# Performance work log

Hardware: AMD Instinct MI355X
Metric: run time of the kernel (lower is better)

## Reference

```python
import jax, jax.numpy as jnp
import numpy as np

N = 100_000      # nodes
E = 1_600_000    # directed edges (avg degree 16)
F_IN = 128       # num_node_features
H = 8            # heads in conv1
C = 32           # hidden_channels
G = 64           # graphs in batch
NC = 10          # num_classes


def setup_inputs() -> dict:
    key = jax.random.key(0)
    ks = jax.random.split(key, 12)
    gl = lambda k, shape, fan: (jax.random.normal(k, shape, jnp.float32) / np.sqrt(fan)).astype(jnp.float32)
    return {
        "x": jax.random.normal(ks[0], (N, F_IN), jnp.float32),
        "edge_index": jax.random.randint(ks[1], (2, E), 0, N, dtype=jnp.int32),
        "batch": jnp.sort(jax.random.randint(ks[2], (N,), 0, G, dtype=jnp.int32)),
        "W1": gl(ks[3], (F_IN, H * C), F_IN),
        "att_src1": gl(ks[4], (H, C), C),
        "att_dst1": gl(ks[5], (H, C), C),
        "b1": jnp.zeros((H * C,), jnp.float32),
        "W2": gl(ks[6], (H * C, C), H * C),
        "att_src2": gl(ks[7], (1, C), C),
        "att_dst2": gl(ks[8], (1, C), C),
        "b2": jnp.zeros((C,), jnp.float32),
        "Wlin": gl(ks[9], (C, NC), C),
        "blin": jnp.zeros((NC,), jnp.float32),
    }


def gat_conv(x, src, dst, W, att_src, att_dst, bias, heads, ch, concat):
    """PyG GATConv (eval mode): gather, LeakyReLU(0.2) scores, segment softmax over dst, scatter-sum."""
    n = x.shape[0]
    h = (x @ W).reshape(n, heads, ch)                     # [N,H,C]
    a_s = jnp.sum(h * att_src, axis=-1)                   # [N,H]
    a_d = jnp.sum(h * att_dst, axis=-1)                   # [N,H]
    e = jax.nn.leaky_relu(a_s[src] + a_d[dst], 0.2)       # [E,H]
    m = jax.ops.segment_max(e, dst, num_segments=n)       # [N,H], stable softmax
    p = jnp.exp(e - m[dst])
    z = jax.ops.segment_sum(p, dst, num_segments=n)
    coef = p / (z[dst] + 1e-16)                           # [E,H]
    out = jax.ops.segment_sum(coef[:, :, None] * h[src], dst, num_segments=n)  # [N,H,C]
    out = out.reshape(n, heads * ch) if concat else out.mean(axis=1)
    return out + bias


def reference(x, edge_index, batch, W1, att_src1, att_dst1, b1,
              W2, att_src2, att_dst2, b2, Wlin, blin):
    n = x.shape[0]
    loops = jnp.arange(n, dtype=edge_index.dtype)         # GATConv add_self_loops=True
    src = jnp.concatenate([edge_index[0], loops])
    dst = jnp.concatenate([edge_index[1], loops])

    h = gat_conv(x, src, dst, W1, att_src1, att_dst1, b1, H, C, concat=True)
    h = jax.nn.elu(h)                                     # dropout is identity in eval
    h = gat_conv(h, src, dst, W2, att_src2, att_dst2, b2, 1, C, concat=False)

    # global_mean_pool over graph ids
    sums = jax.ops.segment_sum(h, batch, num_segments=G)  # [G,C]
    cnts = jax.ops.segment_sum(jnp.ones((n,), h.dtype), batch, num_segments=G)
    pooled = sums / jnp.maximum(cnts, 1.0)[:, None]

    return pooled @ Wlin + blin                           # [G,NC]
```

## Files before the change

kernel.cpp:

```cpp
#include <hip/hip_runtime.h>
#include <cstdint>

#define NN 100000
#define EE 1600000
#define GG 64
#define FIN 128
#define HC 256
#define NC 10

typedef short v8s __attribute__((ext_vector_type(8)));
typedef float v4f __attribute__((ext_vector_type(4)));

static __device__ __forceinline__ float lrelu(float x) { return x > 0.f ? x : 0.2f * x; }
static __device__ __forceinline__ float bf2f(unsigned short b) {
  return __uint_as_float(((unsigned int)b) << 16);
}
static __device__ __forceinline__ unsigned short f2bf(float f) {
  unsigned int u = __float_as_uint(f);
  unsigned int r = (u + 0x7FFFu + ((u >> 16) & 1u)) >> 16;
  return (unsigned short)r;
}
static __device__ __forceinline__ void unpack2(unsigned int u, float& f0, float& f1) {
  f0 = __uint_as_float(u << 16);
  f1 = __uint_as_float(u & 0xFFFF0000u);
}

__global__ __launch_bounds__(256) void k_prep(const int* __restrict__ ei,
                                              int* __restrict__ counts,
                                              const float* __restrict__ W1,
                                              unsigned short* __restrict__ W1tg,
                                              const float* __restrict__ W2,
                                              unsigned short* __restrict__ W2thi,
                                              unsigned short* __restrict__ W2tlo) {
  const int b = blockIdx.x;
  const int t = threadIdx.x;
  if (b < 6250) {
    const int idx = b * 256 + t;
    atomicAdd(&counts[ei[EE + idx]], 1);
  } else if (b < 6506) {
    const int n = b - 6250;
    if (t < 128) W1tg[n * 128 + t] = f2bf(W1[t * HC + n]);
  } else {
    const int oc = b - 6506;
    float wv = W2[t * 32 + oc];
    unsigned short hi = f2bf(wv);
    W2thi[oc * 256 + t] = hi;
    W2tlo[oc * 256 + t] = f2bf(wv - bf2f(hi));
  }
}

__global__ __launch_bounds__(256) void k_gemm1(const float* __restrict__ x,
                                               const unsigned short* __restrict__ W1tg,
                                               const float* __restrict__ att_src1,
                                               const float* __restrict__ att_dst1,
                                               unsigned short* __restrict__ h1b,
                                               float* __restrict__ as1,
                                               float* __restrict__ ad1) {
  const int t = threadIdx.x;
  const int m0 = blockIdx.x * 64;
  const int n0 = blockIdx.y * 128;
  const int hb = blockIdx.y * 4;
  const int lane = t & 63;
  const int wm = t >> 6;
  const int ml = lane & 15;
  const int quad = lane >> 4;
  int row = m0 + wm * 16 + ml; if (row >= NN) row = NN - 1;
  v4f acc[8];
#pragma unroll
  for (int tt = 0; tt < 8; ++tt) acc[tt] = (v4f){0.f, 0.f, 0.f, 0.f};
#pragma unroll
  for (int kk = 0; kk < 4; ++kk) {
    const int k0 = kk * 32 + quad * 8;
    const float4 xa = *(const float4*)(x + (size_t)row * FIN + k0);
    const float4 xc = *(const float4*)(x + (size_t)row * FIN + k0 + 4);
    v8s a;
    a[0] = (short)f2bf(xa.x); a[1] = (short)f2bf(xa.y);
    a[2] = (short)f2bf(xa.z); a[3] = (short)f2bf(xa.w);
    a[4] = (short)f2bf(xc.x); a[5] = (short)f2bf(xc.y);
    a[6] = (short)f2bf(xc.z); a[7] = (short)f2bf(xc.w);
#pragma unroll
    for (int tt = 0; tt < 8; ++tt) {
      v8s b = *(const v8s*)(W1tg + (size_t)(n0 + tt * 16 + ml) * FIN + k0);
      acc[tt] = __builtin_amdgcn_mfma_f32_16x16x32_bf16(a, b, acc[tt], 0, 0, 0);
    }
  }
#pragma unroll
  for (int tt = 0; tt < 8; ++tt) {
#pragma unroll
    for (int r = 0; r < 4; ++r) {
      int rg = m0 + wm * 16 + quad * 4 + r;
      if (rg < NN) h1b[(size_t)rg * HC + n0 + tt * 16 + ml] = f2bf(acc[tt][r]);
    }
  }
  float ps[4][4], pd[4][4];
#pragma unroll
  for (int i = 0; i < 4; ++i)
#pragma unroll
    for (int r = 0; r < 4; ++r) { ps[i][r] = 0.f; pd[i][r] = 0.f; }
#pragma unroll
  for (int i = 0; i < 4; ++i) {
#pragma unroll
    for (int half = 0; half < 2; ++half) {
      const int tt = 2 * i + half;
      const float a_s = att_src1[(hb + i) * 32 + half * 16 + ml];
      const float a_d = att_dst1[(hb + i) * 32 + half * 16 + ml];
#pragma unroll
      for (int r = 0; r < 4; ++r) {
        ps[i][r] += acc[tt][r] * a_s;
        pd[i][r] += acc[tt][r] * a_d;
      }
    }
  }
#pragma unroll
  for (int i = 0; i < 4; ++i) {
#pragma unroll
    for (int r = 0; r < 4; ++r) {
      float s = ps[i][r], d = pd[i][r];
      s += __shfl_xor(s, 1, 64); s += __shfl_xor(s, 2, 64);
      s += __shfl_xor(s, 4, 64); s += __shfl_xor(s, 8, 64);
      d += __shfl_xor(d, 1, 64); d += __shfl_xor(d, 2, 64);
      d += __shfl_xor(d, 4, 64); d += __shfl_xor(d, 8, 64);
      ps[i][r] = s; pd[i][r] = d;
    }
  }
  if (ml == 0) {
#pragma unroll
    for (int r = 0; r < 4; ++r) {
      int rg = m0 + wm * 16 + quad * 4 + r;
      if (rg < NN) {
#pragma unroll
        for (int i = 0; i < 4; ++i) {
          as1[rg * 8 + hb + i] = ps[i][r];
          ad1[rg * 8 + hb + i] = pd[i][r];
        }
      }
    }
  }
}

__global__ void k_scan1(const int* __restrict__ counts, int* __restrict__ offs,
                        int* __restrict__ bsums) {
  __shared__ int s[256];
  const int t = threadIdx.x;
  const int i = blockIdx.x * 256 + t;
  int v = (i < NN) ? counts[i] : 0;
  s[t] = v;
  __syncthreads();
  for (int off = 1; off < 256; off <<= 1) {
    int tv = (t >= off) ? s[t - off] : 0;
    __syncthreads();
    s[t] += tv;
    __syncthreads();
  }
  if (i < NN) offs[i] = s[t] - v;
  if (t == 255) bsums[blockIdx.x] = s[255];
}

__global__ void k_scan2(int* __restrict__ bsums, int nb) {
  __shared__ int s[512];
  const int t = threadIdx.x;
  int v = (t < nb) ? bsums[t] : 0;
  s[t] = v;
  __syncthreads();
  for (int off = 1; off < 512; off <<= 1) {
    int tv = (t >= off) ? s[t - off] : 0;
    __syncthreads();
    s[t] += tv;
    __syncthreads();
  }
  if (t < nb) bsums[t] = s[t] - v;
}

__global__ void k_scan3(int* __restrict__ offs, const int* __restrict__ bsums,
                        int* __restrict__ cursor, int* __restrict__ esrc) {
  const int i = blockIdx.x * 256 + threadIdx.x;
  if (i < NN) {
    int v = offs[i] + bsums[i >> 8];
    offs[i] = v;
    cursor[i] = v;
  }
  if (i == 0) offs[NN] = EE;
  if (blockIdx.x == 0 && threadIdx.x < 16) esrc[EE + threadIdx.x] = 0;
}

__global__ void k_scatter(const int* __restrict__ ei, int* __restrict__ cursor,
                          int* __restrict__ esrc) {
  int e = blockIdx.x * 256 + threadIdx.x;
  if (e < EE) {
    int s = ei[e];
    int d = ei[EE + e];
    int p = atomicAdd(&cursor[d], 1);
    esrc[p] = s;
  }
}

__global__ __launch_bounds__(512) void k_agg1(const unsigned short* __restrict__ h1b,
                                              const float* __restrict__ as1,
                                              const float* __restrict__ ad1,
                                              const int* __restrict__ offs,
                                              const int* __restrict__ esrc,
                                              const float* __restrict__ b1,
                                              const unsigned short* __restrict__ W2thi,
                                              const unsigned short* __restrict__ W2tlo,
                                              const float* __restrict__ att_src2,
                                              const float* __restrict__ att_dst2,
                                              unsigned short* __restrict__ h2b,
                                              float* __restrict__ as2,
                                              float* __restrict__ ad2) {
  __shared__ float wl[8][8][36];
  __shared__ __attribute__((aligned(16))) unsigned short o1hi[8][272];
  __shared__ __attribute__((aligned(16))) unsigned short o1lo[8][272];
  const int t = threadIdx.x;
  const int lane = t & 63;
  const int w = t >> 6;
  const int n0 = blockIdx.x * 8;
  const int nu = __builtin_amdgcn_readfirstlane(n0 + w);
  const int hl = lane & 31;
  const int half = lane >> 5;
  const int head = lane >> 3;
  const uint2* __restrict__ h1u2 = (const uint2*)h1b;
  const int start = offs[nu], end = offs[nu + 1];
  const float4 dnA = *(const float4*)(ad1 + (size_t)nu * 8);
  const float4 dnB = *(const float4*)(ad1 + (size_t)nu * 8 + 4);
  const float4 dn4 = (lane & 32) ? dnB : dnA;

  float z, a0, a1, a2, a3;
  {
    float w0 = __expf(lrelu(as1[nu * 8 + head] + ad1[nu * 8 + head]));
    uint2 q = h1u2[(size_t)nu * 64 + lane];
    float f0, f1, f2, f3; unpack2(q.x, f0, f1); unpack2(q.y, f2, f3);
    z = w0; a0 = w0 * f0; a1 = w0 * f1; a2 = w0 * f2; a3 = w0 * f3;
  }
  for (int base = start; base < end; base += 32) {
    const int cnt = min(32, end - base);
    int s = 0;
    if (hl < cnt) s = esrc[base + hl];
    const int hb4 = half << 2;
    const float4 av = *(const float4*)(as1 + (size_t)s * 8 + hb4);
    float w0 = __expf(lrelu(av.x + dn4.x));
    float w1 = __expf(lrelu(av.y + dn4.y));
    float w2 = __expf(lrelu(av.z + dn4.z));
    float w3 = __expf(lrelu(av.w + dn4.w));
    const bool act = hl < cnt;
    wl[w][hb4 + 0][hl] = act ? w0 : 0.f;
    wl[w][hb4 + 1][hl] = act ? w1 : 0.f;
    wl[w][hb4 + 2][hl] = act ? w2 : 0.f;
    wl[w][hb4 + 3][hl] = act ? w3 : 0.f;
    const int cnt4 = (cnt + 3) & ~3;
    int jb = 0;
    for (; jb + 8 <= cnt4; jb += 8) {
      uint2 q[8];
#pragma unroll
      for (int u = 0; u < 8; ++u) {
        const int sj = esrc[base + jb + u];
        q[u] = h1u2[(size_t)sj * 64 + lane];
      }
      const float4 wq0 = *(const float4*)&wl[w][head][jb];
      const float4 wq1 = *(const float4*)&wl[w][head][jb + 4];
      z += ((wq0.x + wq0.y) + (wq0.z + wq0.w)) + ((wq1.x + wq1.y) + (wq1.z + wq1.w));
      float f0, f1, f2, f3;
      unpack2(q[0].x, f0, f1); unpack2(q[0].y, f2, f3);
      a0 += wq0.x * f0; a1 += wq0.x * f1; a2 += wq0.x * f2; a3 += wq0.x * f3;
      unpack2(q[1].x, f0, f1); unpack2(q[1].y, f2, f3);
      a0 += wq0.y * f0; a1 += wq0.y * f1; a2 += wq0.y * f2; a3 += wq0.y * f3;
      unpack2(q[2].x, f0, f1); unpack2(q[2].y, f2, f3);
      a0 += wq0.z * f0; a1 += wq0.z * f1; a2 += wq0.z * f2; a3 += wq0.z * f3;
      unpack2(q[3].x, f0, f1); unpack2(q[3].y, f2, f3);
      a0 += wq0.w * f0; a1 += wq0.w * f1; a2 += wq0.w * f2; a3 += wq0.w * f3;
      unpack2(q[4].x, f0, f1); unpack2(q[4].y, f2, f3);
      a0 += wq1.x * f0; a1 += wq1.x * f1; a2 += wq1.x * f2; a3 += wq1.x * f3;
      unpack2(q[5].x, f0, f1); unpack2(q[5].y, f2, f3);
      a0 += wq1.y * f0; a1 += wq1.y * f1; a2 += wq1.y * f2; a3 += wq1.y * f3;
      unpack2(q[6].x, f0, f1); unpack2(q[6].y, f2, f3);
      a0 += wq1.z * f0; a1 += wq1.z * f1; a2 += wq1.z * f2; a3 += wq1.z * f3;
      unpack2(q[7].x, f0, f1); unpack2(q[7].y, f2, f3);
      a0 += wq1.w * f0; a1 += wq1.w * f1; a2 += wq1.w * f2; a3 += wq1.w * f3;
    }
    if (jb < cnt4) {
      uint2 q[4];
#pragma unroll
      for (int u = 0; u < 4; ++u) {
        const int sj = esrc[base + jb + u];
        q[u] = h1u2[(size_t)sj * 64 + lane];
      }
      const float4 wq0 = *(const float4*)&wl[w][head][jb];
      z += (wq0.x + wq0.y) + (wq0.z + wq0.w);
      float f0, f1, f2, f3;
      unpack2(q[0].x, f0, f1); unpack2(q[0].y, f2, f3);
      a0 += wq0.x * f0; a1 += wq0.x * f1; a2 += wq0.x * f2; a3 += wq0.x * f3;
      unpack2(q[1].x, f0, f1); unpack2(q[1].y, f2, f3);
      a0 += wq0.y * f0; a1 += wq0.y * f1; a2 += wq0.y * f2; a3 += wq0.y * f3;
      unpack2(q[2].x, f0, f1); unpack2(q[2].y, f2, f3);
      a0 += wq0.z * f0; a1 += wq0.z * f1; a2 += wq0.z * f2; a3 += wq0.z * f3;
      unpack2(q[3].x, f0, f1); unpack2(q[3].y, f2, f3);
      a0 += wq0.w * f0; a1 += wq0.w * f1; a2 += wq0.w * f2; a3 += wq0.w * f3;
    }
  }
  {
    const float zi = 1.0f / (z + 1e-16f);
    const float4 bb = *(const float4*)(b1 + 4 * lane);
    float v0 = a0 * zi + bb.x;
    float v1 = a1 * zi + bb.y;
    float v2 = a2 * zi + bb.z;
    float v3 = a3 * zi + bb.w;
    v0 = v0 > 0.f ? v0 : (__expf(v0) - 1.0f);
    v1 = v1 > 0.f ? v1 : (__expf(v1) - 1.0f);
    v2 = v2 > 0.f ? v2 : (__expf(v2) - 1.0f);
    v3 = v3 > 0.f ? v3 : (__expf(v3) - 1.0f);
    ushort4 hh, ll;
    hh.x = f2bf(v0); hh.y = f2bf(v1); hh.z = f2bf(v2); hh.w = f2bf(v3);
    ll.x = f2bf(v0 - bf2f(hh.x));
    ll.y = f2bf(v1 - bf2f(hh.y));
    ll.z = f2bf(v2 - bf2f(hh.z));
    ll.w = f2bf(v3 - bf2f(hh.w));
    *(ushort4*)&o1hi[w][4 * lane] = hh;
    *(ushort4*)&o1lo[w][4 * lane] = ll;
  }
  __syncthreads();
  if (w == 0) {
    const int ml = lane & 15;
    const int quad = lane >> 4;
    const int mr = ml & 7;
    v4f acc[2];
    acc[0] = (v4f){0.f, 0.f, 0.f, 0.f};
    acc[1] = (v4f){0.f, 0.f, 0.f, 0.f};
#pragma unroll
    for (int kk = 0; kk < 8; ++kk) {
      const int k0 = kk * 32 + quad * 8;
      v8s ah = *(const v8s*)&o1hi[mr][k0];
      v8s al = *(const v8s*)&o1lo[mr][k0];
#pragma unroll
      for (int tt = 0; tt < 2; ++tt) {
        v8s bh = *(const v8s*)(W2thi + (size_t)(tt * 16 + ml) * 256 + k0);
        v8s bl = *(const v8s*)(W2tlo + (size_t)(tt * 16 + ml) * 256 + k0);
        acc[tt] = __builtin_amdgcn_mfma_f32_16x16x32_bf16(ah, bh, acc[tt], 0, 0, 0);
        acc[tt] = __builtin_amdgcn_mfma_f32_16x16x32_bf16(al, bh, acc[tt], 0, 0, 0);
        acc[tt] = __builtin_amdgcn_mfma_f32_16x16x32_bf16(ah, bl, acc[tt], 0, 0, 0);
      }
    }
    if (quad < 2) {
      const float s0 = att_src2[ml], s1 = att_src2[16 + ml];
      const float d0 = att_dst2[ml], d1 = att_dst2[16 + ml];
#pragma unroll
      for (int r = 0; r < 4; ++r) {
        const int nn = n0 + quad * 4 + r;
        const float h0 = acc[0][r], h1v = acc[1][r];
        h2b[(size_t)nn * 32 + ml] = f2bf(h0);
        h2b[(size_t)nn * 32 + 16 + ml] = f2bf(h1v);
        float ps = h0 * s0 + h1v * s1;
        float pd = h0 * d0 + h1v * d1;
        ps += __shfl_xor(ps, 1, 64); ps += __shfl_xor(ps, 2, 64);
        ps += __shfl_xor(ps, 4, 64); ps += __shfl_xor(ps, 8, 64);
        pd += __shfl_xor(pd, 1, 64); pd += __shfl_xor(pd, 2, 64);
        pd += __shfl_xor(pd, 4, 64); pd += __shfl_xor(pd, 8, 64);
        if (ml == 0) { as2[nn] = ps; ad2[nn] = pd; }
      }
    }
  }
}

__global__ __launch_bounds__(256) void k_agg2(const unsigned short* __restrict__ h2b,
                                              const float* __restrict__ as2,
                                              const float* __restrict__ ad2,
                                              const int* __restrict__ offs,
                                              const int* __restrict__ esrc,
                                              const float* __restrict__ b2,
                                              float* __restrict__ h3) {
  __shared__ int2 swl[4][64];
  const int t = threadIdx.x;
  const int lane = t & 63;
  const int wv = t >> 6;
  const int n = __builtin_amdgcn_readfirstlane(blockIdx.x * 4 + wv);
  const int col = lane & 15;
  const int slot = lane >> 4;
  const unsigned int* __restrict__ h2u = (const unsigned int*)h2b;
  const int start = offs[n], end = offs[n + 1];
  const float adn = ad2[n];
  float z = 0.f, acc0 = 0.f, acc1 = 0.f;
  if (slot == 0) {
    float w0 = __expf(lrelu(as2[n] + adn));
    unsigned int q = h2u[(unsigned)(n * 16 + col)];
    float f0, f1; unpack2(q, f0, f1);
    z = w0; acc0 = w0 * f0; acc1 = w0 * f1;
  }
  for (int base = start; base < end; base += 64) {
    const int cnt = min(64, end - base);
    int s = 0; float wgt = 0.f;
    if (lane < cnt) {
      s = esrc[base + lane];
      wgt = __expf(lrelu(as2[s] + adn));
    }
    swl[wv][lane] = make_int2(s, __float_as_int(wgt));
    const int nit = (cnt + 7) >> 3;
#pragma unroll 2
    for (int j = 0; j < nit; ++j) {
      const int2 p0 = swl[wv][8 * j + slot];
      const int2 p1 = swl[wv][8 * j + 4 + slot];
      const unsigned int q0 = h2u[(unsigned)(p0.x * 16 + col)];
      const unsigned int q1 = h2u[(unsigned)(p1.x * 16 + col)];
      const float wj0 = __int_as_float(p0.y);
      const float wj1 = __int_as_float(p1.y);
      float f0, f1, g0, g1;
      unpack2(q0, f0, f1); unpack2(q1, g0, g1);
      z += wj0 + wj1;
      acc0 += wj0 * f0; acc0 += wj1 * g0;
      acc1 += wj0 * f1; acc1 += wj1 * g1;
    }
  }
  acc0 += __shfl_xor(acc0, 16, 64); acc0 += __shfl_xor(acc0, 32, 64);
  acc1 += __shfl_xor(acc1, 16, 64); acc1 += __shfl_xor(acc1, 32, 64);
  z    += __shfl_xor(z, 16, 64);    z    += __shfl_xor(z, 32, 64);
  if (slot == 0) {
    const float zi = 1.0f / (z + 1e-16f);
    float2 bb = *(const float2*)(b2 + 2 * col);
    float2 o;
    o.x = acc0 * zi + bb.x;
    o.y = acc1 * zi + bb.y;
    *(float2*)(h3 + (size_t)n * 32 + 2 * col) = o;
  }
}

__global__ __launch_bounds__(256) void k_poolfin(const float* __restrict__ h3,
                                                 const int* __restrict__ batch,
                                                 const float* __restrict__ Wlin,
                                                 const float* __restrict__ blin,
                                                 float* __restrict__ out) {
  __shared__ int bounds[2];
  __shared__ float red[8][33];
  __shared__ float mean[32];
  const int g = blockIdx.x;
  const int t = threadIdx.x;
  if (t < 2) {
    int target = g + t;
    int lo = 0, hi = NN;
    while (lo < hi) { int mid = (lo + hi) >> 1; if (batch[mid] < target) lo = mid + 1; else hi = mid; }
    bounds[t] = lo;
  }
  __syncthreads();
  const int lo = bounds[0], hi = bounds[1];
  const int rr = t >> 5, c = t & 31;
  float a = 0.f;
  for (int r = lo + rr; r < hi; r += 8) a += h3[(size_t)r * 32 + c];
  red[rr][c] = a;
  __syncthreads();
  if (rr == 0) {
    float s = 0.f;
#pragma unroll
    for (int i = 0; i < 8; ++i) s += red[i][c];
    float ct = (float)(hi - lo);
    ct = ct > 1.f ? ct : 1.f;
    mean[c] = s / ct;
  }
  __syncthreads();
  if (t < NC) {
    float acc = 0.f;
#pragma unroll
    for (int cc = 0; cc < 32; ++cc) acc += mean[cc] * Wlin[cc * NC + t];
    out[g * NC + t] = acc + blin[t];
  }
}

extern "C" void kernel_launch(void* const* d_in, const int* in_sizes, int n_in,
                              void* d_out, int out_size, void* d_ws, size_t ws_size,
                              hipStream_t stream) {
  const float* x        = (const float*)d_in[0];
  const int*   ei       = (const int*)d_in[1];
  const int*   batch    = (const int*)d_in[2];
  const float* W1       = (const float*)d_in[3];
  const float* att_src1 = (const float*)d_in[4];
  const float* att_dst1 = (const float*)d_in[5];
  const float* b1       = (const float*)d_in[6];
  const float* W2       = (const float*)d_in[7];
  const float* att_src2 = (const float*)d_in[8];
  const float* att_dst2 = (const float*)d_in[9];
  const float* b2       = (const float*)d_in[10];
  const float* Wlin     = (const float*)d_in[11];
  const float* blin     = (const float*)d_in[12];
  float* out = (float*)d_out;
  char* ws = (char*)d_ws;

  unsigned short* h1b   = (unsigned short*)(ws + 0);
  float* as1    = (float*)(ws + 51200000);
  float* ad1    = (float*)(ws + 54400000);
  int* counts   = (int*)(ws + 57600000);
  int* offs     = (int*)(ws + 58000000);
  int* cursor   = (int*)(ws + 58400256);
  int* esrc     = (int*)(ws + 58800256);
  int* bsums    = (int*)(ws + 65200384);
  unsigned short* h2b   = (unsigned short*)(ws + 65202048);
  float* as2    = (float*)(ws + 71602048);
  float* ad2    = (float*)(ws + 72002048);
  unsigned short* W1tg  = (unsigned short*)(ws + 72402048);
  unsigned short* W2thi = (unsigned short*)(ws + 72467584);
  unsigned short* W2tlo = (unsigned short*)(ws + 72483968);
  float* h3     = (float*)(ws + 72500352);

  const int nb_scan = (NN + 255) / 256;

  hipMemsetAsync(counts, 0, NN * sizeof(int), stream);
  k_prep<<<6538, 256, 0, stream>>>(ei, counts, W1, W1tg, W2, W2thi, W2tlo);

  dim3 g1((NN + 63) / 64, 2);
  k_gemm1<<<g1, 256, 0, stream>>>(x, W1tg, att_src1, att_dst1, h1b, as1, ad1);

  k_scan1<<<nb_scan, 256, 0, stream>>>(counts, offs, bsums);
  k_scan2<<<1, 512, 0, stream>>>(bsums, nb_scan);
  k_scan3<<<nb_scan, 256, 0, stream>>>(offs, bsums, cursor, esrc);
  k_scatter<<<(EE + 255) / 256, 256, 0, stream>>>(ei, cursor, esrc);

  k_agg1<<<NN / 8, 512, 0, stream>>>(h1b, as1, ad1, offs, esrc, b1, W2thi, W2tlo,
                                     att_src2, att_dst2, h2b, as2, ad2);

  k_agg2<<<NN / 4, 256, 0, stream>>>(h2b, as2, ad2, offs, esrc, b2, h3);
  k_poolfin<<<GG, 256, 0, stream>>>(h3, batch, Wlin, blin, out);
}
```

Baseline: 582.2 us.

## Fuse mean-pool into agg2 via atomics and widen gemm1 to full 256 columns

k_agg2 no longer writes the per-node h3 array. It atomically accumulates each node's output into a per-graph pooled buffer, and a small k_fin kernel divides by the node counts and applies the linear layer. This removes the h3 write and re-read and the pool reduction kernel, at the cost of heavy atomic contention on only 64×32 addresses. Separately, gemm1 now computes all 256 output columns in one block instead of splitting them across two y-blocks, so x is loaded and converted once per row. That raises accumulator register use to 16 v4f per thread and may lower occupancy.

After: 776.2 us. 33.3% more time.

```diff
diff --git a/kernel.cpp b/kernel.cpp
--- a/kernel.cpp
+++ b/kernel.cpp
@@ -58,16 +58,14 @@
                                                float* __restrict__ ad1) {
   const int t = threadIdx.x;
   const int m0 = blockIdx.x * 64;
-  const int n0 = blockIdx.y * 128;
-  const int hb = blockIdx.y * 4;
   const int lane = t & 63;
   const int wm = t >> 6;
   const int ml = lane & 15;
   const int quad = lane >> 4;
   int row = m0 + wm * 16 + ml; if (row >= NN) row = NN - 1;
-  v4f acc[8];
-#pragma unroll
-  for (int tt = 0; tt < 8; ++tt) acc[tt] = (v4f){0.f, 0.f, 0.f, 0.f};
+  v4f acc[16];
+#pragma unroll
+  for (int tt = 0; tt < 16; ++tt) acc[tt] = (v4f){0.f, 0.f, 0.f, 0.f};
 #pragma unroll
   for (int kk = 0; kk < 4; ++kk) {
     const int k0 = kk * 32 + quad * 8;
@@ -79,60 +77,45 @@
     a[4] = (short)f2bf(xc.x); a[5] = (short)f2bf(xc.y);
     a[6] = (short)f2bf(xc.z); a[7] = (short)f2bf(xc.w);
 #pragma unroll
-    for (int tt = 0; tt < 8; ++tt) {
-      v8s b = *(const v8s*)(W1tg + (size_t)(n0 + tt * 16 + ml) * FIN + k0);
+    for (int tt = 0; tt < 16; ++tt) {
+      v8s b = *(const v8s*)(W1tg + (size_t)(tt * 16 + ml) * FIN + k0);
       acc[tt] = __builtin_amdgcn_mfma_f32_16x16x32_bf16(a, b, acc[tt], 0, 0, 0);
     }
   }
 #pragma unroll
-  for (int tt = 0; tt < 8; ++tt) {
+  for (int tt = 0; tt < 16; ++tt) {
 #pragma unroll
     for (int r = 0; r < 4; ++r) {
       int rg = m0 + wm * 16 + quad * 4 + r;
-      if (rg < NN) h1b[(size_t)rg * HC + n0 + tt * 16 + ml] = f2bf(acc[tt][r]);
-    }
-  }
-  float ps[4][4], pd[4][4];
-#pragma unroll
-  for (int i = 0; i < 4; ++i)
-#pragma unroll
-    for (int r = 0; r < 4; ++r) { ps[i][r] = 0.f; pd[i][r] = 0.f; }
-#pragma unroll
-  for (int i = 0; i < 4; ++i) {
+      if (rg < NN) h1b[(size_t)rg * HC + tt * 16 + ml] = f2bf(acc[tt][r]);
+    }
+  }
+#pragma unroll
+  for (int i = 0; i < 8; ++i) {
+    float ps[4], pd[4];
+#pragma unroll
+    for (int r = 0; r < 4; ++r) { ps[r] = 0.f; pd[r] = 0.f; }
 #pragma unroll
     for (int half = 0; half < 2; ++half) {
       const int tt = 2 * i + half;
-      const float a_s = att_src1[(hb + i) * 32 + half * 16 + ml];
-      const float a_d = att_dst1[(hb + i) * 32 + half * 16 + ml];
+      const float a_s = att_src1[i * 32 + half * 16 + ml];
+      const float a_d = att_dst1[i * 32 + half * 16 + ml];
 #pragma unroll
       for (int r = 0; r < 4; ++r) {
-        ps[i][r] += acc[tt][r] * a_s;
-        pd[i][r] += acc[tt][r] * a_d;
-      }
-    }
-  }
-#pragma unroll
-  for (int i = 0; i < 4; ++i) {
+        ps[r] += acc[tt][r] * a_s;
+        pd[r] += acc[tt][r] * a_d;
+      }
+    }
 #pragma unroll
     for (int r = 0; r < 4; ++r) {
-      float s = ps[i][r], d = pd[i][r];
+      float s = ps[r], d = pd[r];
       s += __shfl_xor(s, 1, 64); s += __shfl_xor(s, 2, 64);
       s += __shfl_xor(s, 4, 64); s += __shfl_xor(s, 8, 64);
       d += __shfl_xor(d, 1, 64); d += __shfl_xor(d, 2, 64);
       d += __shfl_xor(d, 4, 64); d += __shfl_xor(d, 8, 64);
-      ps[i][r] = s; pd[i][r] = d;
-    }
-  }
-  if (ml == 0) {
-#pragma unroll
-    for (int r = 0; r < 4; ++r) {
-      int rg = m0 + wm * 16 + quad * 4 + r;
-      if (rg < NN) {
-#pragma unroll
-        for (int i = 0; i < 4; ++i) {
-          as1[rg * 8 + hb + i] = ps[i][r];
-          ad1[rg * 8 + hb + i] = pd[i][r];
-        }
+      if (ml == 0) {
+        int rg = m0 + wm * 16 + quad * 4 + r;
+        if (rg < NN) { as1[rg * 8 + i] = s; ad1[rg * 8 + i] = d; }
       }
     }
   }
@@ -365,7 +348,8 @@
                                               const int* __restrict__ offs,
                                               const int* __restrict__ esrc,
                                               const float* __restrict__ b2,
-                                              float* __restrict__ h3) {
+                                              const int* __restrict__ batch,
+                                              float* __restrict__ pooled) {
   __shared__ int2 swl[4][64];
   const int t = threadIdx.x;
   const int lane = t & 63;
@@ -413,20 +397,18 @@
   if (slot == 0) {
     const float zi = 1.0f / (z + 1e-16f);
     float2 bb = *(const float2*)(b2 + 2 * col);
-    float2 o;
-    o.x = acc0 * zi + bb.x;
-    o.y = acc1 * zi + bb.y;
-    *(float2*)(h3 + (size_t)n * 32 + 2 * col) = o;
-  }
-}
-
-__global__ __launch_bounds__(256) void k_poolfin(const float* __restrict__ h3,
-                                                 const int* __restrict__ batch,
-                                                 const float* __restrict__ Wlin,
-                                                 const float* __restrict__ blin,
-                                                 float* __restrict__ out) {
+    const int g = batch[n];
+    atomicAdd(&pooled[g * 32 + 2 * col],     acc0 * zi + bb.x);
+    atomicAdd(&pooled[g * 32 + 2 * col + 1], acc1 * zi + bb.y);
+  }
+}
+
+__global__ __launch_bounds__(64) void k_fin(const float* __restrict__ pooled,
+                                            const int* __restrict__ batch,
+                                            const float* __restrict__ Wlin,
+                                            const float* __restrict__ blin,
+                                            float* __restrict__ out) {
   __shared__ int bounds[2];
-  __shared__ float red[8][33];
   __shared__ float mean[32];
   const int g = blockIdx.x;
   const int t = threadIdx.x;
@@ -437,19 +419,10 @@
     bounds[t] = lo;
   }
   __syncthreads();
-  const int lo = bounds[0], hi = bounds[1];
-  const int rr = t >> 5, c = t & 31;
-  float a = 0.f;
-  for (int r = lo + rr; r < hi; r += 8) a += h3[(size_t)r * 32 + c];
-  red[rr][c] = a;
-  __syncthreads();
-  if (rr == 0) {
-    float s = 0.f;
-#pragma unroll
-    for (int i = 0; i < 8; ++i) s += red[i][c];
-    float ct = (float)(hi - lo);
+  if (t < 32) {
+    float ct = (float)(bounds[1] - bounds[0]);
     ct = ct > 1.f ? ct : 1.f;
-    mean[c] = s / ct;
+    mean[t] = pooled[g * 32 + t] / ct;
   }
   __syncthreads();
   if (t < NC) {
@@ -483,25 +456,24 @@
   float* as1    = (float*)(ws + 51200000);
   float* ad1    = (float*)(ws + 54400000);
   int* counts   = (int*)(ws + 57600000);
-  int* offs     = (int*)(ws + 58000000);
-  int* cursor   = (int*)(ws + 58400256);
-  int* esrc     = (int*)(ws + 58800256);
-  int* bsums    = (int*)(ws + 65200384);
-  unsigned short* h2b   = (unsigned short*)(ws + 65202048);
-  float* as2    = (float*)(ws + 71602048);
-  float* ad2    = (float*)(ws + 72002048);
-  unsigned short* W1tg  = (unsigned short*)(ws + 72402048);
-  unsigned short* W2thi = (unsigned short*)(ws + 72467584);
-  unsigned short* W2tlo = (unsigned short*)(ws + 72483968);
-  float* h3     = (float*)(ws + 72500352);
+  float* pooled = (float*)(ws + 58000000);
+  int* offs     = (int*)(ws + 58008192);
+  int* cursor   = (int*)(ws + 58408448);
+  int* esrc     = (int*)(ws + 58808448);
+  int* bsums    = (int*)(ws + 65208512);
+  unsigned short* h2b   = (unsigned short*)(ws + 65210112);
+  float* as2    = (float*)(ws + 71610112);
+  float* ad2    = (float*)(ws + 72010112);
+  unsigned short* W1tg  = (unsigned short*)(ws + 72410112);
+  unsigned short* W2thi = (unsigned short*)(ws + 72475648);
+  unsigned short* W2tlo = (unsigned short*)(ws + 72492032);
 
   const int nb_scan = (NN + 255) / 256;
 
-  hipMemsetAsync(counts, 0, NN * sizeof(int), stream);
+  hipMemsetAsync(counts, 0, 408192, stream);
   k_prep<<<6538, 256, 0, stream>>>(ei, counts, W1, W1tg, W2, W2thi, W2tlo);
 
-  dim3 g1((NN + 63) / 64, 2);
-  k_gemm1<<<g1, 256, 0, stream>>>(x, W1tg, att_src1, att_dst1, h1b, as1, ad1);
+  k_gemm1<<<(NN + 63) / 64, 256, 0, stream>>>(x, W1tg, att_src1, att_dst1, h1b, as1, ad1);
 
   k_scan1<<<nb_scan, 256, 0, stream>>>(counts, offs, bsums);
   k_scan2<<<1, 512, 0, stream>>>(bsums, nb_scan);
@@ -511,6 +483,6 @@
   k_agg1<<<NN / 8, 512, 0, stream>>>(h1b, as1, ad1, offs, esrc, b1, W2thi, W2tlo,
                                      att_src2, att_dst2, h2b, as2, ad2);
 
-  k_agg2<<<NN / 4, 256, 0, stream>>>(h2b, as2, ad2, offs, esrc, b2, h3);
-  k_poolfin<<<GG, 256, 0, stream>>>(h3, batch, Wlin, blin, out);
-}
+  k_agg2<<<NN / 4, 256, 0, stream>>>(h2b, as2, ad2, offs, esrc, b2, batch, pooled);
+  k_fin<<<GG, 64, 0, stream>>>(pooled, batch, Wlin, blin, out);
+}
```
